# Kernel tuning notes

Measured on AMD Instinct MI355X. Metric: run time of the kernel, lower is better.

The kernel has to match this reference:

```python
import jax, jax.numpy as jnp
import numpy as np

B, W, C_BLK, N_EMBD, N_HEADS = 512, 128, 24, 32, 2


def setup_inputs() -> dict:
    key = jax.random.key(0)
    k1, k2, k3, k4 = jax.random.split(key, 4)
    x = jax.random.normal(k1, (B, W, C_BLK, N_EMBD), dtype=jnp.float32)
    x_end_idx = jax.random.randint(k2, (B, W), 0, C_BLK, dtype=jnp.int32)
    # nn.Linear(n_embd, 3*n_embd, bias=False): store transposed so y = x @ w
    w_attn = jax.random.normal(k3, (N_EMBD, 3 * N_EMBD), dtype=jnp.float32) * (1.0 / np.sqrt(N_EMBD))
    w_proj = jax.random.normal(k4, (N_EMBD, N_EMBD), dtype=jnp.float32) * (1.0 / np.sqrt(N_EMBD))
    return {"x": x, "x_end_idx": x_end_idx, "w_attn": w_attn, "w_proj": w_proj}


def reference(x, x_end_idx, w_attn, w_proj):
    # x: [B, W, c, C]; causal self-attention over the char axis c, per (batch, word).
    Bd, Wd, c, C = x.shape
    H = N_HEADS
    D = C // H
    qkv = x @ w_attn                               # [B, W, c, 3C]
    q, k, v = jnp.split(qkv, 3, axis=-1)
    # [B, W, H, c, D]
    q = q.reshape(Bd, Wd, c, H, D).transpose(0, 1, 3, 2, 4)
    k = k.reshape(Bd, Wd, c, H, D).transpose(0, 1, 3, 2, 4)
    v = v.reshape(Bd, Wd, c, H, D).transpose(0, 1, 3, 2, 4)
    scale = 1.0 / jnp.sqrt(jnp.asarray(D, dtype=x.dtype))
    scores = jnp.einsum('bwhqd,bwhkd->bwhqk', q, k) * scale   # [B, W, H, c, c]
    causal = jnp.tril(jnp.ones((c, c), dtype=bool))
    scores = jnp.where(causal, scores, jnp.asarray(-jnp.inf, dtype=scores.dtype))
    att = jax.nn.softmax(scores, axis=-1)
    out = jnp.einsum('bwhqk,bwhkd->bwhqd', att, v)            # [B, W, H, c, D]
    out = out.transpose(0, 1, 3, 2, 4).reshape(Bd, Wd, c, C)
    out = out @ w_proj                                        # c_proj (dropout in eval mode = identity)
    out = x + out                                             # residual
    # Vectorized last-token gather: pick out[b, w, x_end_idx[b, w], :]
    idx = x_end_idx[:, :, None, None].astype(jnp.int32)       # [B, W, 1, 1]
    samples = jnp.take_along_axis(out, jnp.broadcast_to(idx, (Bd, Wd, 1, C)), axis=2)
    return samples.squeeze(2)                                 # [B, W, C]
```

## Files before the change

### kernel.cpp

```cpp
#include <hip/hip_runtime.h>


#define CB      24
#define CC      32
#define DD      16
#define THREEC  96
#define NBW     (512 * 128)
#define WPB     4
#define XSS     34

__device__ __align__(16) float g_Mt[2][CC][CC];
__device__ __align__(16) float g_Pt[2][CC][CC];

__global__ void precompute_mp(const float* __restrict__ w_attn,
                              const float* __restrict__ w_proj)
{
    const int idx = blockIdx.x * 256 + threadIdx.x;
    const int h = idx >> 10, c = (idx >> 5) & 31, e = idx & 31;
    float m = 0.f, p = 0.f;
    #pragma unroll
    for (int d = 0; d < DD; ++d) {
        const int i = DD * h + d;
        m = fmaf(w_attn[e * THREEC + i],          w_attn[c * THREEC + CC + i], m);
        p = fmaf(w_attn[e * THREEC + 2 * CC + i], w_proj[i * CC + c],          p);
    }
    g_Mt[h][c][e] = 0.25f * m;
    g_Pt[h][c][e] = p;
}

struct __align__(16) WaveSmem {
    float xs[CB][XSS];
    float rks[2][CC];
    float ps[2][CC];
    float ys[2][CC];
};

__device__ __forceinline__ void wave_fence() {
    __asm__ volatile("s_waitcnt lgkmcnt(0)" ::: "memory");
}

__global__ __launch_bounds__(256, 8) void char_attn_kernel(
    const float* __restrict__ x,
    const int*   __restrict__ xend,
    float*       __restrict__ out)
{
    __shared__ WaveSmem sm[WPB];

    const int tid  = threadIdx.x;
    const int lane = tid & 63;
    const int wave = tid >> 6;
    WaveSmem& S = sm[wave];

    const int bid  = blockIdx.x * WPB + wave;
    const int i32  = lane & 31;
    const int half = lane >> 5;

    const int qidx = xend[bid];
    const int L    = qidx + 1;
    const float* xb = x + (size_t)bid * (CB * CC);

    {
        const float2* xb2 = (const float2*)xb;
        const int n2 = L * (CC / 2);
        #pragma unroll
        for (int t0 = 0; t0 < CB * (CC / 2); t0 += 64) {
            const int t = t0 + lane;
            float2 v = make_float2(0.f, 0.f);
            if (t < n2) v = xb2[t];
            const int r = t >> 4, c = (t & 15) * 2;
            *(float2*)&S.xs[r][c] = v;
        }
    }
    wave_fence();

    {
        const float4* m4 = (const float4*)&g_Mt[half][i32][0];
        float a0 = 0.f, a1 = 0.f, a2 = 0.f, a3 = 0.f;
        #pragma unroll
        for (int e4 = 0; e4 < 8; ++e4) {
            const float4 mv = m4[e4];
            const float2 x0 = *(const float2*)&S.xs[qidx][e4 * 4];
            const float2 x1 = *(const float2*)&S.xs[qidx][e4 * 4 + 2];
            a0 = fmaf(mv.x, x0.x, a0);
            a1 = fmaf(mv.y, x0.y, a1);
            a2 = fmaf(mv.z, x1.x, a2);
            a3 = fmaf(mv.w, x1.y, a3);
        }
        S.rks[half][i32] = (a0 + a1) + (a2 + a3);
    }
    wave_fence();

    {
        float sc = -INFINITY;
        if (i32 <= qidx) {
            float a0 = 0.f, a1 = 0.f;
            #pragma unroll
            for (int c = 0; c < CC; c += 2) {
                const float2 xv = *(const float2*)&S.xs[i32][c];
                const float2 rv = *(const float2*)&S.rks[half][c];
                a0 = fmaf(xv.x, rv.x, a0);
                a1 = fmaf(xv.y, rv.y, a1);
            }
            sc = a0 + a1;
        }
        float m = sc;
        #pragma unroll
        for (int off = 16; off >= 1; off >>= 1)
            m = fmaxf(m, __shfl_xor(m, off));
        const float e = (i32 <= qidx) ? __expf(sc - m) : 0.f;
        float sum = e;
        #pragma unroll
        for (int off = 16; off >= 1; off >>= 1)
            sum += __shfl_xor(sum, off);
        S.ps[half][i32] = __fdividef(e, sum);
    }
    wave_fence();

    {
        float a0 = 0.f, a1 = 0.f;
        #pragma unroll
        for (int j = 0; j < CB; j += 2) {
            const float2 p2 = *(const float2*)&S.ps[half][j];
            a0 = fmaf(p2.x, S.xs[j][i32],     a0);
            a1 = fmaf(p2.y, S.xs[j + 1][i32], a1);
        }
        S.ys[half][i32] = a0 + a1;
    }
    wave_fence();

    {
        const float4* p4 = (const float4*)&g_Pt[half][i32][0];
        float a0 = 0.f, a1 = 0.f, a2 = 0.f, a3 = 0.f;
        #pragma unroll
        for (int e4 = 0; e4 < 8; ++e4) {
            const float4 pv = p4[e4];
            const float2 y0 = *(const float2*)&S.ys[half][e4 * 4];
            const float2 y1 = *(const float2*)&S.ys[half][e4 * 4 + 2];
            a0 = fmaf(pv.x, y0.x, a0);
            a1 = fmaf(pv.y, y0.y, a1);
            a2 = fmaf(pv.z, y1.x, a2);
            a3 = fmaf(pv.w, y1.y, a3);
        }
        float t = (a0 + a1) + (a2 + a3);
        t += __shfl_xor(t, 32);
        if (lane < CC)
            out[(size_t)bid * CC + i32] = t + S.xs[qidx][i32];
    }
}

extern "C" void kernel_launch(void* const* d_in, const int* in_sizes, int n_in,
                              void* d_out, int out_size, void* d_ws, size_t ws_size,
                              hipStream_t stream) {
    const float* x      = (const float*)d_in[0];
    const int*   xend   = (const int*)d_in[1];
    const float* w_attn = (const float*)d_in[2];
    const float* w_proj = (const float*)d_in[3];
    float* out = (float*)d_out;

    precompute_mp<<<dim3(8), dim3(256), 0, stream>>>(w_attn, w_proj);
    char_attn_kernel<<<dim3(NBW / WPB), dim3(WPB * 64), 0, stream>>>(
        x, xend, out);
}
```

Baseline: 346.3 us.

## Read x directly from global memory instead of staging through LDS

```diff
diff --git a/kernel.cpp b/kernel.cpp
--- a/kernel.cpp
+++ b/kernel.cpp
@@ -7,7 +7,6 @@
 #define THREEC  96
 #define NBW     (512 * 128)
 #define WPB     4
-#define XSS     34
 
 __device__ __align__(16) float g_Mt[2][CC][CC];
 __device__ __align__(16) float g_Pt[2][CC][CC];
@@ -29,7 +28,6 @@
 }
 
 struct __align__(16) WaveSmem {
-    float xs[CB][XSS];
     float rks[2][CC];
     float ps[2][CC];
     float ys[2][CC];
@@ -51,27 +49,15 @@
     const int wave = tid >> 6;
     WaveSmem& S = sm[wave];
 
-    const int bid  = blockIdx.x * WPB + wave;
     const int i32  = lane & 31;
     const int half = lane >> 5;
 
-    const int qidx = xend[bid];
-    const int L    = qidx + 1;
-    const float* xb = x + (size_t)bid * (CB * CC);
+    const int sbid = __builtin_amdgcn_readfirstlane(blockIdx.x * WPB + wave);
+    const int sq   = __builtin_amdgcn_readfirstlane(xend[sbid]);
+    const int L    = sq + 1;
 
-    {
-        const float2* xb2 = (const float2*)xb;
-        const int n2 = L * (CC / 2);
-        #pragma unroll
-        for (int t0 = 0; t0 < CB * (CC / 2); t0 += 64) {
-            const int t = t0 + lane;
-            float2 v = make_float2(0.f, 0.f);
-            if (t < n2) v = xb2[t];
-            const int r = t >> 4, c = (t & 15) * 2;
-            *(float2*)&S.xs[r][c] = v;
-        }
-    }
-    wave_fence();
+    const float* __restrict__ xb = x + (size_t)sbid * (CB * CC);
+    const float* __restrict__ xq = xb + sq * CC;
 
     {
         const float4* m4 = (const float4*)&g_Mt[half][i32][0];
@@ -79,12 +65,11 @@
         #pragma unroll
         for (int e4 = 0; e4 < 8; ++e4) {
             const float4 mv = m4[e4];
-            const float2 x0 = *(const float2*)&S.xs[qidx][e4 * 4];
-            const float2 x1 = *(const float2*)&S.xs[qidx][e4 * 4 + 2];
-            a0 = fmaf(mv.x, x0.x, a0);
-            a1 = fmaf(mv.y, x0.y, a1);
-            a2 = fmaf(mv.z, x1.x, a2);
-            a3 = fmaf(mv.w, x1.y, a3);
+            const float4 xv = *(const float4*)(xq + e4 * 4);
+            a0 = fmaf(mv.x, xv.x, a0);
+            a1 = fmaf(mv.y, xv.y, a1);
+            a2 = fmaf(mv.z, xv.z, a2);
+            a3 = fmaf(mv.w, xv.w, a3);
         }
         S.rks[half][i32] = (a0 + a1) + (a2 + a3);
     }
@@ -92,22 +77,26 @@
 
     {
         float sc = -INFINITY;
-        if (i32 <= qidx) {
-            float a0 = 0.f, a1 = 0.f;
+        if (i32 <= sq) {
+            const float4* xr  = (const float4*)(xb + i32 * CC);
+            const float4* rk4 = (const float4*)&S.rks[half][0];
+            float a0 = 0.f, a1 = 0.f, a2 = 0.f, a3 = 0.f;
             #pragma unroll
-            for (int c = 0; c < CC; c += 2) {
-                const float2 xv = *(const float2*)&S.xs[i32][c];
-                const float2 rv = *(const float2*)&S.rks[half][c];
-                a0 = fmaf(xv.x, rv.x, a0);
-                a1 = fmaf(xv.y, rv.y, a1);
+            for (int e4 = 0; e4 < 8; ++e4) {
+                const float4 rv = rk4[e4];
+                const float4 xv = xr[e4];
+                a0 = fmaf(rv.x, xv.x, a0);
+                a1 = fmaf(rv.y, xv.y, a1);
+                a2 = fmaf(rv.z, xv.z, a2);
+                a3 = fmaf(rv.w, xv.w, a3);
             }
-            sc = a0 + a1;
+            sc = (a0 + a1) + (a2 + a3);
         }
         float m = sc;
         #pragma unroll
         for (int off = 16; off >= 1; off >>= 1)
             m = fmaxf(m, __shfl_xor(m, off));
-        const float e = (i32 <= qidx) ? __expf(sc - m) : 0.f;
+        const float e = (i32 <= sq) ? __expf(sc - m) : 0.f;
         float sum = e;
         #pragma unroll
         for (int off = 16; off >= 1; off >>= 1)
@@ -118,33 +107,35 @@
 
     {
         float a0 = 0.f, a1 = 0.f;
-        #pragma unroll
-        for (int j = 0; j < CB; j += 2) {
+        int j = 0;
+        for (; j + 1 < L; j += 2) {
             const float2 p2 = *(const float2*)&S.ps[half][j];
-            a0 = fmaf(p2.x, S.xs[j][i32],     a0);
-            a1 = fmaf(p2.y, S.xs[j + 1][i32], a1);
+            a0 = fmaf(p2.x, xb[j * CC + i32],       a0);
+            a1 = fmaf(p2.y, xb[(j + 1) * CC + i32], a1);
         }
+        if (j < L)
+            a0 = fmaf(S.ps[half][j], xb[j * CC + i32], a0);
         S.ys[half][i32] = a0 + a1;
     }
     wave_fence();
 
     {
         const float4* p4 = (const float4*)&g_Pt[half][i32][0];
+        const float4* y4 = (const float4*)&S.ys[half][0];
         float a0 = 0.f, a1 = 0.f, a2 = 0.f, a3 = 0.f;
         #pragma unroll
         for (int e4 = 0; e4 < 8; ++e4) {
             const float4 pv = p4[e4];
-            const float2 y0 = *(const float2*)&S.ys[half][e4 * 4];
-            const float2 y1 = *(const float2*)&S.ys[half][e4 * 4 + 2];
-            a0 = fmaf(pv.x, y0.x, a0);
-            a1 = fmaf(pv.y, y0.y, a1);
-            a2 = fmaf(pv.z, y1.x, a2);
-            a3 = fmaf(pv.w, y1.y, a3);
+            const float4 yv = y4[e4];
+            a0 = fmaf(pv.x, yv.x, a0);
+            a1 = fmaf(pv.y, yv.y, a1);
+            a2 = fmaf(pv.z, yv.z, a2);
+            a3 = fmaf(pv.w, yv.w, a3);
         }
         float t = (a0 + a1) + (a2 + a3);
         t += __shfl_xor(t, 32);
         if (lane < CC)
-            out[(size_t)bid * CC + i32] = t + S.xs[qidx][i32];
+            out[(size_t)sbid * CC + i32] = t + xq[i32];
     }
 }
 
```

Result: slower. 378.2 us (+9.2%).
